# Kernel optimization log

Measured on AMD Instinct MI355X. Metric: run time of the kernel, lower is better.

The kernel has to match this reference:

```python
import jax, jax.numpy as jnp
import numpy as np

N, M, D = 131072, 2048, 2


def setup_inputs() -> dict:
    key = jax.random.key(0)
    k1, k2 = jax.random.split(key)
    sample = jax.random.normal(k1, (N, D), dtype=jnp.float32)
    mu = jax.random.uniform(k2, (M, D), dtype=jnp.float32)
    # A initialized as 15 * I per component, exactly as in the torch module
    A = (15.0 * jnp.broadcast_to(jnp.eye(D, dtype=jnp.float32), (M, D, D))).astype(jnp.float32)
    w = jnp.ones((M, 1), dtype=jnp.float32)
    return {"sample": sample, "mu": mu, "A": A, "w": w}


def reference(sample, mu, A, w):
    """GaussianMixture.log_likelihoods(sample): logsumexp_j( wlog_j - (x-mu_j)^T G_j (x-mu_j) )."""
    # update_covariances: G_m = A_m A_m^T / 2, shape (M, D, D)
    G = jnp.einsum('mij,mkj->mik', A, A) * 0.5
    g00, g01, g10, g11 = G[:, 0, 0], G[:, 0, 1], G[:, 1, 0], G[:, 1, 1]  # (M,)
    # covariances_determinants (2x2 case) + weights_log
    dets = g00 * g11 - g01 * g10                                          # (M,)
    wlog = jax.nn.log_softmax(w, axis=0)[:, 0] + 0.5 * jnp.log(dets)      # (M,)
    # Pairwise Mahalanobis quadratic form, D=2 expanded to avoid an (N,M,D) temp
    dx0 = sample[:, 0:1] - mu[None, :, 0]   # (N, M)
    dx1 = sample[:, 1:2] - mu[None, :, 1]   # (N, M)
    q = g00 * dx0 * dx0 + (g01 + g10) * dx0 * dx1 + g11 * dx1 * dx1       # (N, M)
    # mode='lse' reduction of kernel_product: log sum_j exp(wlog_j - q_ij)
    ll = jax.nn.logsumexp(wlog[None, :] - q, axis=1, keepdims=True)       # (N, 1)
    return ll
```

## Files before the change

kernel.cpp:

```cpp
#include <hip/hip_runtime.h>
#include <math.h>


#if __has_builtin(__builtin_amdgcn_exp2f)
#define EXP2(x) __builtin_amdgcn_exp2f(x)
#else
#define EXP2(x) exp2f(x)
#endif

typedef float v2f __attribute__((ext_vector_type(2)));

#if __has_builtin(__builtin_elementwise_max)
#define PKMAX(a, b) __builtin_elementwise_max(a, b)
#else
static __device__ inline v2f PKMAX(v2f a, v2f b) {
  v2f r; r.x = fmaxf(a.x, b.x); r.y = fmaxf(a.y, b.y); return r;
}
#endif

#define SPLIT 4
#define YSPLIT 4
#define CH 16

__global__ __launch_bounds__(256) void prep_kernel(
    const float* __restrict__ mu,
    const float* __restrict__ A,
    const float* __restrict__ w,
    float* __restrict__ C,
    int M) {
  __shared__ float red[256];
  __shared__ int uni[256];
  const int t = threadIdx.x;

  float mx = -INFINITY;
  for (int m = t; m < M; m += 256) mx = fmaxf(mx, w[m]);
  red[t] = mx; __syncthreads();
  for (int s = 128; s > 0; s >>= 1) {
    if (t < s) red[t] = fmaxf(red[t], red[t + s]);
    __syncthreads();
  }
  const float wmax = red[0]; __syncthreads();

  float sum = 0.f;
  for (int m = t; m < M; m += 256) sum += expf(w[m] - wmax);
  red[t] = sum; __syncthreads();
  for (int s = 128; s > 0; s >>= 1) {
    if (t < s) red[t] += red[t + s];
    __syncthreads();
  }
  const float logZ = wmax + logf(red[0]);

  const float r00 = A[0], r01 = A[1], r10 = A[2], r11 = A[3];
  const float rg00 = 0.5f * (r00 * r00 + r01 * r01);
  const float rg01 = 0.5f * (r00 * r10 + r01 * r11);
  const float rg11 = 0.5f * (r10 * r10 + r11 * r11);

  const float LOG2E = 1.44269504088896340736f;
  int myuni = 1;
  for (int m = t; m < M; m += 256) {
    const float a00 = A[m * 4 + 0], a01 = A[m * 4 + 1];
    const float a10 = A[m * 4 + 2], a11 = A[m * 4 + 3];
    const float g00 = 0.5f * (a00 * a00 + a01 * a01);
    const float g01 = 0.5f * (a00 * a10 + a01 * a11);
    const float g11 = 0.5f * (a10 * a10 + a11 * a11);
    const float g01s = 2.0f * g01;
    const float det = g00 * g11 - g01 * g01;
    const float wlog = (w[m] - logZ) + 0.5f * logf(det);
    const float mu0 = mu[m * 2 + 0], mu1 = mu[m * 2 + 1];
    const float c0 = wlog - (g00 * mu0 * mu0 + g01s * mu0 * mu1 + g11 * mu1 * mu1);
    const float c2 = 2.0f * g00 * mu0 + g01s * mu1;
    const float c4 = 2.0f * g11 * mu1 + g01s * mu0;
    C[0 * M + m] = LOG2E * c0;
    C[1 * M + m] = LOG2E * -g00;
    C[2 * M + m] = LOG2E * c2;
    C[3 * M + m] = LOG2E * -g11;
    C[4 * M + m] = LOG2E * c4;
    C[5 * M + m] = LOG2E * -g01s;
    myuni &= (g00 == rg00) & (g01 == rg01) & (g11 == rg11);
  }
  uni[t] = myuni; __syncthreads();
  for (int s = 128; s > 0; s >>= 1) {
    if (t < s) uni[t] &= uni[t + s];
    __syncthreads();
  }
  if (t == 0) {
    ((int*)C)[6 * M + 0] = uni[0];
    C[6 * M + 1] = LOG2E * -rg00;
    C[6 * M + 2] = LOG2E * -rg11;
    C[6 * M + 3] = LOG2E * -2.0f * rg01;
  }
}

__global__ __launch_bounds__(256) void gmix_kernel(
    const float* __restrict__ sample,
    const float* __restrict__ C,
    float* __restrict__ P,
    int N, int M) {
  __shared__ float Lmx[SPLIT][2][64];
  __shared__ float Lsm[SPLIT][2][64];

  const int lane = threadIdx.x & 63;
  const int wave = __builtin_amdgcn_readfirstlane((int)(threadIdx.x >> 6));
  const int nA = blockIdx.x * 128 + lane;
  const int nB = nA + 64;

  const float2 xA = (nA < N) ? ((const float2*)sample)[nA] : make_float2(0.f, 0.f);
  const float2 xB = (nB < N) ? ((const float2*)sample)[nB] : make_float2(0.f, 0.f);
  const v2f x0p = {xA.x, xB.x};
  const v2f x1p = {xA.y, xB.y};

  const int flag = ((const int*)C)[6 * M + 0];
  const float cb1 = C[6 * M + 1];
  const float cb3 = C[6 * M + 2];
  const float cb5 = C[6 * M + 3];

  const int Mq = M / (SPLIT * YSPLIT);
  const int m0 = (blockIdx.y * SPLIT + wave) * Mq;
  const float* __restrict__ C0 = C + m0;
  const float* __restrict__ C1 = C + M + m0;
  const float* __restrict__ C2 = C + 2 * M + m0;
  const float* __restrict__ C3 = C + 3 * M + m0;
  const float* __restrict__ C4 = C + 4 * M + m0;
  const float* __restrict__ C5 = C + 5 * M + m0;

  v2f basep = {0.f, 0.f};
  float mxA = -INFINITY, sA = 0.0f;
  float mxB = -INFINITY, sB = 0.0f;

  if (flag) {
    basep = cb1 * x0p * x0p + cb3 * x1p * x1p + cb5 * x0p * x1p;
    for (int m = 0; m < Mq; m += CH) {
      v2f a[CH];
#pragma unroll
      for (int j = 0; j < CH; ++j) {
        const float c0 = C0[m + j], c2 = C2[m + j], c4 = C4[m + j];
        v2f t = x0p * c2 + c0;
        a[j] = x1p * c4 + t;
      }
      v2f cm01 = PKMAX(a[0], a[1]);
      v2f cm23 = PKMAX(a[2], a[3]);
      v2f cm45 = PKMAX(a[4], a[5]);
      v2f cm67 = PKMAX(a[6], a[7]);
#pragma unroll
      for (int j = 8; j < CH; j += 4) {
        cm01 = PKMAX(cm01, a[j]);
        cm23 = PKMAX(cm23, a[j + 1]);
        cm45 = PKMAX(cm45, a[j + 2]);
        cm67 = PKMAX(cm67, a[j + 3]);
      }
      const v2f cm = PKMAX(PKMAX(cm01, cm23), PKMAX(cm45, cm67));
      const float nmA = fmaxf(mxA, cm.x);
      const float nmB = fmaxf(mxB, cm.y);
      sA *= EXP2(mxA - nmA);
      sB *= EXP2(mxB - nmB);
      const v2f nmp = {nmA, nmB};
      float lA0 = 0.f, lA1 = 0.f, lB0 = 0.f, lB1 = 0.f;
#pragma unroll
      for (int j = 0; j < CH; j += 2) {
        const v2f d0 = a[j] - nmp;
        const v2f d1 = a[j + 1] - nmp;
        lA0 += EXP2(d0.x);
        lB0 += EXP2(d0.y);
        lA1 += EXP2(d1.x);
        lB1 += EXP2(d1.y);
      }
      sA += lA0 + lA1; mxA = nmA;
      sB += lB0 + lB1; mxB = nmB;
    }
  } else {
    for (int m = 0; m < Mq; m += CH) {
      v2f a[CH];
#pragma unroll
      for (int j = 0; j < CH; ++j) {
        const float c0 = C0[m + j], c1 = C1[m + j], c2 = C2[m + j];
        const float c3 = C3[m + j], c4 = C4[m + j], c5 = C5[m + j];
        v2f t0 = x0p * c1 + c2;
        t0 = x1p * c5 + t0;
        v2f t1 = x1p * c3 + c4;
        v2f r = t0 * x0p + c0;
        a[j] = t1 * x1p + r;
      }
      v2f cm01 = PKMAX(a[0], a[1]);
      v2f cm23 = PKMAX(a[2], a[3]);
      v2f cm45 = PKMAX(a[4], a[5]);
      v2f cm67 = PKMAX(a[6], a[7]);
#pragma unroll
      for (int j = 8; j < CH; j += 4) {
        cm01 = PKMAX(cm01, a[j]);
        cm23 = PKMAX(cm23, a[j + 1]);
        cm45 = PKMAX(cm45, a[j + 2]);
        cm67 = PKMAX(cm67, a[j + 3]);
      }
      const v2f cm = PKMAX(PKMAX(cm01, cm23), PKMAX(cm45, cm67));
      const float nmA = fmaxf(mxA, cm.x);
      const float nmB = fmaxf(mxB, cm.y);
      sA *= EXP2(mxA - nmA);
      sB *= EXP2(mxB - nmB);
      const v2f nmp = {nmA, nmB};
      float lA0 = 0.f, lA1 = 0.f, lB0 = 0.f, lB1 = 0.f;
#pragma unroll
      for (int j = 0; j < CH; j += 2) {
        const v2f d0 = a[j] - nmp;
        const v2f d1 = a[j + 1] - nmp;
        lA0 += EXP2(d0.x);
        lB0 += EXP2(d0.y);
        lA1 += EXP2(d1.x);
        lB1 += EXP2(d1.y);
      }
      sA += lA0 + lA1; mxA = nmA;
      sB += lB0 + lB1; mxB = nmB;
    }
  }

  Lmx[wave][0][lane] = mxA + basep.x; Lsm[wave][0][lane] = sA;
  Lmx[wave][1][lane] = mxB + basep.y; Lsm[wave][1][lane] = sB;
  __syncthreads();

  if (wave < 2) {
    const int set = wave;
    const int n = blockIdx.x * 128 + set * 64 + lane;
    if (n < N) {
      float gm = Lmx[0][set][lane];
#pragma unroll
      for (int v = 1; v < SPLIT; ++v) gm = fmaxf(gm, Lmx[v][set][lane]);
      float S = 0.f;
#pragma unroll
      for (int v = 0; v < SPLIT; ++v)
        S += Lsm[v][set][lane] * EXP2(Lmx[v][set][lane] - gm);
      P[blockIdx.y * N + n] = gm + __log2f(S);
    }
  }
}

__global__ __launch_bounds__(256) void combine_kernel(
    const float* __restrict__ P,
    float* __restrict__ out,
    int N) {
  const int n = blockIdx.x * blockDim.x + threadIdx.x;
  if (n >= N) return;
  float p0 = P[0 * N + n];
  float p1 = P[1 * N + n];
  float p2 = P[2 * N + n];
  float p3 = P[3 * N + n];
  float mx = fmaxf(fmaxf(p0, p1), fmaxf(p2, p3));
  float S = EXP2(p0 - mx) + EXP2(p1 - mx) + EXP2(p2 - mx) + EXP2(p3 - mx);
  out[n] = (mx + __log2f(S)) * 0.69314718055994530942f;
}

extern "C" void kernel_launch(void* const* d_in, const int* in_sizes, int n_in,
                              void* d_out, int out_size, void* d_ws, size_t ws_size,
                              hipStream_t stream) {
  const float* sample = (const float*)d_in[0];
  const float* mu     = (const float*)d_in[1];
  const float* A      = (const float*)d_in[2];
  const float* w      = (const float*)d_in[3];
  float* out = (float*)d_out;

  const int N = in_sizes[0] / 2;
  const int M = in_sizes[3];

  float* C = (float*)d_ws;
  float* P = (float*)d_ws + 6 * M + 16;

  prep_kernel<<<1, 256, 0, stream>>>(mu, A, w, C, M);
  dim3 grid((N + 127) / 128, YSPLIT);
  gmix_kernel<<<grid, 256, 0, stream>>>(sample, C, P, N, M);
  combine_kernel<<<(N + 255) / 256, 256, 0, stream>>>(P, out, N);
}
```

Baseline: 110.5 us.

## Double the M-split, parallelize prep, and fully unroll the uniform-covariance loop

Splits the component dimension across 8 grid rows instead of 4, so each wave handles a shorter M range. The combine kernel now merges 8 partial results per point. Prep writes its coefficient tables from 8 blocks, while block 0 alone still runs the uniformity check over all of M. The uniform path's loop is hardcoded to 64 iterations and fully unrolled, with the coefficient loads hoisted ahead of the math; this only matches M=2048 and doubles the partial-result traffic through P.

```diff
diff --git a/kernel.cpp b/kernel.cpp
--- a/kernel.cpp
+++ b/kernel.cpp
@@ -19,7 +19,7 @@
 #endif
 
 #define SPLIT 4
-#define YSPLIT 4
+#define YSPLIT 8
 #define CH 16
 
 __global__ __launch_bounds__(256) void prep_kernel(
@@ -29,7 +29,6 @@
     float* __restrict__ C,
     int M) {
   __shared__ float red[256];
-  __shared__ int uni[256];
   const int t = threadIdx.x;
 
   float mx = -INFINITY;
@@ -50,14 +49,10 @@
   }
   const float logZ = wmax + logf(red[0]);
 
-  const float r00 = A[0], r01 = A[1], r10 = A[2], r11 = A[3];
-  const float rg00 = 0.5f * (r00 * r00 + r01 * r01);
-  const float rg01 = 0.5f * (r00 * r10 + r01 * r11);
-  const float rg11 = 0.5f * (r10 * r10 + r11 * r11);
-
   const float LOG2E = 1.44269504088896340736f;
-  int myuni = 1;
-  for (int m = t; m < M; m += 256) {
+  const int Ms = M / gridDim.x;
+  const int mlo = blockIdx.x * Ms, mhi = mlo + Ms;
+  for (int m = mlo + t; m < mhi; m += 256) {
     const float a00 = A[m * 4 + 0], a01 = A[m * 4 + 1];
     const float a10 = A[m * 4 + 2], a11 = A[m * 4 + 3];
     const float g00 = 0.5f * (a00 * a00 + a01 * a01);
@@ -76,18 +71,34 @@
     C[3 * M + m] = LOG2E * -g11;
     C[4 * M + m] = LOG2E * c4;
     C[5 * M + m] = LOG2E * -g01s;
-    myuni &= (g00 == rg00) & (g01 == rg01) & (g11 == rg11);
-  }
-  uni[t] = myuni; __syncthreads();
-  for (int s = 128; s > 0; s >>= 1) {
-    if (t < s) uni[t] &= uni[t + s];
-    __syncthreads();
-  }
-  if (t == 0) {
-    ((int*)C)[6 * M + 0] = uni[0];
-    C[6 * M + 1] = LOG2E * -rg00;
-    C[6 * M + 2] = LOG2E * -rg11;
-    C[6 * M + 3] = LOG2E * -2.0f * rg01;
+  }
+
+  if (blockIdx.x == 0) {
+    __shared__ int uni[256];
+    const float r00 = A[0], r01 = A[1], r10 = A[2], r11 = A[3];
+    const float rg00 = 0.5f * (r00 * r00 + r01 * r01);
+    const float rg01 = 0.5f * (r00 * r10 + r01 * r11);
+    const float rg11 = 0.5f * (r10 * r10 + r11 * r11);
+    int myuni = 1;
+    for (int m = t; m < M; m += 256) {
+      const float a00 = A[m * 4 + 0], a01 = A[m * 4 + 1];
+      const float a10 = A[m * 4 + 2], a11 = A[m * 4 + 3];
+      const float g00 = 0.5f * (a00 * a00 + a01 * a01);
+      const float g01 = 0.5f * (a00 * a10 + a01 * a11);
+      const float g11 = 0.5f * (a10 * a10 + a11 * a11);
+      myuni &= (g00 == rg00) & (g01 == rg01) & (g11 == rg11);
+    }
+    uni[t] = myuni; __syncthreads();
+    for (int s = 128; s > 0; s >>= 1) {
+      if (t < s) uni[t] &= uni[t + s];
+      __syncthreads();
+    }
+    if (t == 0) {
+      ((int*)C)[6 * M + 0] = uni[0];
+      C[6 * M + 1] = LOG2E * -rg00;
+      C[6 * M + 2] = LOG2E * -rg11;
+      C[6 * M + 3] = LOG2E * -2.0f * rg01;
+    }
   }
 }
 
@@ -129,13 +140,18 @@
 
   if (flag) {
     basep = cb1 * x0p * x0p + cb3 * x1p * x1p + cb5 * x0p * x1p;
-    for (int m = 0; m < Mq; m += CH) {
+#pragma unroll
+    for (int m = 0; m < 64; m += CH) {
+      float c0r[CH], c2r[CH], c4r[CH];
+#pragma unroll
+      for (int j = 0; j < CH; ++j) {
+        c0r[j] = C0[m + j]; c2r[j] = C2[m + j]; c4r[j] = C4[m + j];
+      }
       v2f a[CH];
 #pragma unroll
       for (int j = 0; j < CH; ++j) {
-        const float c0 = C0[m + j], c2 = C2[m + j], c4 = C4[m + j];
-        v2f t = x0p * c2 + c0;
-        a[j] = x1p * c4 + t;
+        v2f t = x0p * c2r[j] + c0r[j];
+        a[j] = x1p * c4r[j] + t;
       }
       v2f cm01 = PKMAX(a[0], a[1]);
       v2f cm23 = PKMAX(a[2], a[3]);
@@ -238,13 +254,19 @@
     int N) {
   const int n = blockIdx.x * blockDim.x + threadIdx.x;
   if (n >= N) return;
-  float p0 = P[0 * N + n];
-  float p1 = P[1 * N + n];
-  float p2 = P[2 * N + n];
-  float p3 = P[3 * N + n];
-  float mx = fmaxf(fmaxf(p0, p1), fmaxf(p2, p3));
-  float S = EXP2(p0 - mx) + EXP2(p1 - mx) + EXP2(p2 - mx) + EXP2(p3 - mx);
-  out[n] = (mx + __log2f(S)) * 0.69314718055994530942f;
+  float p[YSPLIT];
+#pragma unroll
+  for (int y = 0; y < YSPLIT; ++y) p[y] = P[y * N + n];
+  float mx = p[0];
+#pragma unroll
+  for (int y = 1; y < YSPLIT; ++y) mx = fmaxf(mx, p[y]);
+  float S0 = 0.f, S1 = 0.f;
+#pragma unroll
+  for (int y = 0; y < YSPLIT; y += 2) {
+    S0 += EXP2(p[y] - mx);
+    S1 += EXP2(p[y + 1] - mx);
+  }
+  out[n] = (mx + __log2f(S0 + S1)) * 0.69314718055994530942f;
 }
 
 extern "C" void kernel_launch(void* const* d_in, const int* in_sizes, int n_in,
@@ -262,7 +284,7 @@
   float* C = (float*)d_ws;
   float* P = (float*)d_ws + 6 * M + 16;
 
-  prep_kernel<<<1, 256, 0, stream>>>(mu, A, w, C, M);
+  prep_kernel<<<8, 256, 0, stream>>>(mu, A, w, C, M);
   dim3 grid((N + 127) / 128, YSPLIT);
   gmix_kernel<<<grid, 256, 0, stream>>>(sample, C, P, N, M);
   combine_kernel<<<(N + 255) / 256, 256, 0, stream>>>(P, out, N);
```

Measured after the change: 110.5 us. Within noise of the previous version (-0.0%).
